# Kernel tuning notes

Measured on AMD Instinct MI355X. Metric: run time of the kernel, lower is better.

Reference implementation:

```python
import jax, jax.numpy as jnp
import numpy as np

D_MODEL = 1024
N_HEADS = 16
N_EXPERTS = 8
TOP_K = 2
EXPERT_HIDDEN = D_MODEL * 4 // N_EXPERTS  # 512, per MoELayer default


def layer_norm(x, g, b, eps=1e-5):
    mu = jnp.mean(x, axis=-1, keepdims=True)
    var = jnp.var(x, axis=-1, keepdims=True)
    return (x - mu) * jax.lax.rsqrt(var + eps) * g + b


def setup_inputs() -> dict:
    key = jax.random.key(0)
    ks = jax.random.split(key, 12)
    s = 1.0 / np.sqrt(D_MODEL)
    return {
        "x": jax.random.normal(ks[0], (2, 2048, D_MODEL), dtype=jnp.float32),
        "Wq": jax.random.normal(ks[1], (D_MODEL, D_MODEL), dtype=jnp.float32) * s,
        "Wk": jax.random.normal(ks[2], (D_MODEL, D_MODEL), dtype=jnp.float32) * s,
        "Wv": jax.random.normal(ks[3], (D_MODEL, D_MODEL), dtype=jnp.float32) * s,
        "Wo": jax.random.normal(ks[4], (D_MODEL, D_MODEL), dtype=jnp.float32) * s,
        "g1": jnp.ones((D_MODEL,), jnp.float32),
        "b1": jnp.zeros((D_MODEL,), jnp.float32),
        "g2": jnp.ones((D_MODEL,), jnp.float32),
        "b2": jnp.zeros((D_MODEL,), jnp.float32),
        "Wg": jax.random.normal(ks[5], (D_MODEL, N_EXPERTS), dtype=jnp.float32) * s,
        "W1": jax.random.normal(ks[6], (N_EXPERTS, D_MODEL, EXPERT_HIDDEN), dtype=jnp.float32) * s,
        "W2": jax.random.normal(ks[7], (N_EXPERTS, EXPERT_HIDDEN, D_MODEL), dtype=jnp.float32) * (1.0 / np.sqrt(EXPERT_HIDDEN)),
    }


def reference(x, Wq, Wk, Wv, Wo, g1, b1, g2, b2, Wg, W1, W2):
    B, S, D = x.shape
    H, dk = N_HEADS, D // N_HEADS

    # ---- pre-norm attention + residual (dropout = identity in eval) ----
    xn = layer_norm(x, g1, b1)
    q = (xn @ Wq).reshape(B, S, H, dk).transpose(0, 2, 1, 3)  # [B,H,S,dk]
    k = (xn @ Wk).reshape(B, S, H, dk).transpose(0, 2, 1, 3)
    v = (xn @ Wv).reshape(B, S, H, dk).transpose(0, 2, 1, 3)
    scores = jnp.einsum("bhqd,bhkd->bhqk", q, k) / np.sqrt(dk)
    attn = jax.nn.softmax(scores, axis=-1)
    o = jnp.einsum("bhqk,bhkd->bhqd", attn, v)
    o = o.transpose(0, 2, 1, 3).reshape(B, S, D) @ Wo
    x = x + o

    # ---- pre-norm MoE + residual ----
    xn2 = layer_norm(x, g2, b2)
    xf = xn2.reshape(B * S, D)  # [T, D]
    gate = xf @ Wg  # [T, E]
    topv, topi = jax.lax.top_k(gate, TOP_K)  # [T, K]
    probs = jax.nn.softmax(topv, axis=-1)    # softmax over top-k scores
    # dense combine weights [T, E] (top-k indices are distinct)
    cw = jnp.sum(jax.nn.one_hot(topi, N_EXPERTS, dtype=xf.dtype) * probs[..., None], axis=1)
    h = jax.nn.relu(jnp.einsum("td,edh->teh", xf, W1))  # [T,E,Hid]
    y = jnp.einsum("teh,ehd->ted", h, W2)               # [T,E,D]
    moe = jnp.einsum("ted,te->td", y, cw).reshape(B, S, D)
    return x + moe
```

## Files before the change

### kernel.cpp

```cpp
#include <hip/hip_runtime.h>

typedef __attribute__((ext_vector_type(8))) _Float16 f16x8;
typedef __attribute__((ext_vector_type(4))) _Float16 f16x4;
typedef __attribute__((ext_vector_type(2))) _Float16 f16x2;
typedef __attribute__((ext_vector_type(2))) __fp16 fp16x2_n;
typedef __attribute__((ext_vector_type(8))) short bf16x8;
typedef __attribute__((ext_vector_type(4))) float f32x4;
typedef __attribute__((ext_vector_type(4))) unsigned short u16x4;
typedef __attribute__((ext_vector_type(4))) float fx4;

#define D_MODEL 1024
#define N_HEADS 16
#define SEQ 2048
#define TOKENS 4096
#define N_EXP 8
#define EHID 512
#define LO_S 2048.0f
#define INV_LO (1.0f / 2048.0f)
#define QSCALE 0.18033688011112043f
#define DTHR 11.0f

__device__ inline unsigned short f2bf(float f) {
  union { float f; unsigned u; } v; v.f = f;
  unsigned u = v.u;
  return (unsigned short)((u + 0x7FFFu + ((u >> 16) & 1u)) >> 16);
}

__device__ inline void split16(float v, _Float16& h, _Float16& l) {
  h = (_Float16)v;
  l = (_Float16)((v - (float)h) * LO_S);
}

__device__ inline void split2(float a, float b, f16x2& h, f16x2& l) {
  fp16x2_n hn = __builtin_amdgcn_cvt_pkrtz(a, b);
  h = __builtin_bit_cast(f16x2, hn);
  fp16x2_n ln = __builtin_amdgcn_cvt_pkrtz((a - (float)h[0]) * LO_S, (b - (float)h[1]) * LO_S);
  l = __builtin_bit_cast(f16x2, ln);
}

__device__ inline void gload_lds16(const void* g, void* lds) {
  __builtin_amdgcn_global_load_lds((const __attribute__((address_space(1))) void*)g,
                                   (__attribute__((address_space(3))) void*)lds, 16, 0, 0);
}

__global__ __launch_bounds__(256) void prep_kernel(const float* __restrict__ Wq, const float* __restrict__ Wk,
                                                   const float* __restrict__ Wv, const float* __restrict__ Wo,
                                                   const float* __restrict__ W1, const float* __restrict__ W2,
                                                   _Float16* __restrict__ qkvh, _Float16* __restrict__ qkvl,
                                                   _Float16* __restrict__ woh, _Float16* __restrict__ wol,
                                                   unsigned short* __restrict__ W1T, unsigned short* __restrict__ W2T,
                                                   int* __restrict__ cnt, int* __restrict__ perm) {
  int b = blockIdx.x;
  if (b >= 12288) {
    int i = (b - 12288) * 256 + threadIdx.x;
    if (i < 8) cnt[i] = 0;
    if (i < 8704) perm[i] = 0;
    return;
  }
  __shared__ float tile[32][33];
  int tx = threadIdx.x & 31, ty = threadIdx.x >> 5;
  if (b < 4096) {
    int z = b >> 10, rem = b & 1023;
    int c0 = (rem & 31) * 32, r0 = (rem >> 5) * 32;
    const float* src = (z == 0) ? Wq : (z == 1) ? Wk : (z == 2) ? Wv : Wo;
    _Float16* dh = (z < 3) ? qkvh + (size_t)z * 1048576 : woh;
    _Float16* dl = (z < 3) ? qkvl + (size_t)z * 1048576 : wol;
    #pragma unroll
    for (int i = 0; i < 4; i++) tile[ty + 8*i][tx] = src[(size_t)(r0 + ty + 8*i) * 1024 + c0 + tx];
    __syncthreads();
    #pragma unroll
    for (int i = 0; i < 4; i++) {
      float v = tile[tx][ty + 8*i];
      _Float16 h, lo; split16(v, h, lo);
      size_t idx = (size_t)(c0 + ty + 8*i) * 1024 + r0 + tx;
      dh[idx] = h; dl[idx] = lo;
    }
  } else if (b < 8192) {
    int q = b - 4096, z = q >> 9, rem = q & 511;
    int c0 = (rem & 15) * 32, r0 = (rem >> 4) * 32;
    const float* src = W1 + (size_t)z * 524288;
    unsigned short* dst = W1T + (size_t)z * 524288;
    #pragma unroll
    for (int i = 0; i < 4; i++) tile[ty + 8*i][tx] = src[(size_t)(r0 + ty + 8*i) * 512 + c0 + tx];
    __syncthreads();
    #pragma unroll
    for (int i = 0; i < 4; i++) dst[(size_t)(c0 + ty + 8*i) * 1024 + r0 + tx] = f2bf(tile[tx][ty + 8*i]);
  } else {
    int q = b - 8192, z = q >> 9, rem = q & 511;
    int c0 = (rem & 31) * 32, r0 = (rem >> 5) * 32;
    const float* src = W2 + (size_t)z * 524288;
    unsigned short* dst = W2T + (size_t)z * 524288;
    #pragma unroll
    for (int i = 0; i < 4; i++) tile[ty + 8*i][tx] = src[(size_t)(r0 + ty + 8*i) * 1024 + c0 + tx];
    __syncthreads();
    #pragma unroll
    for (int i = 0; i < 4; i++) dst[(size_t)(c0 + ty + 8*i) * 512 + r0 + tx] = f2bf(tile[tx][ty + 8*i]);
  }
}

__global__ __launch_bounds__(256) void ln_f16s_kernel(const float* __restrict__ x, const float* __restrict__ g,
                                                      const float* __restrict__ b,
                                                      _Float16* __restrict__ xh, _Float16* __restrict__ xl) {
  int t = blockIdx.x, tid = threadIdx.x;
  const float* row = x + (size_t)t * D_MODEL;
  fx4 v = *(const fx4*)(row + tid * 4);
  float s = v[0] + v[1] + v[2] + v[3];
  float s2 = v[0]*v[0] + v[1]*v[1] + v[2]*v[2] + v[3]*v[3];
  #pragma unroll
  for (int off = 1; off < 64; off <<= 1) { s += __shfl_xor(s, off); s2 += __shfl_xor(s2, off); }
  __shared__ float red[8];
  int wv = tid >> 6, wl = tid & 63;
  if (wl == 0) { red[wv] = s; red[4 + wv] = s2; }
  __syncthreads();
  s = red[0] + red[1] + red[2] + red[3];
  s2 = red[4] + red[5] + red[6] + red[7];
  float mu = s * (1.f / 1024.f);
  float var = s2 * (1.f / 1024.f) - mu * mu;
  float rstd = rsqrtf(var + 1e-5f);
  int kk = tid * 4;
  f16x4 oh, ol;
  #pragma unroll
  for (int c = 0; c < 4; c++) {
    float y = (v[c] - mu) * rstd * g[kk + c] + b[kk + c];
    _Float16 h, lo; split16(y, h, lo);
    oh[c] = h; ol[c] = lo;
  }
  *(f16x4*)(xh + (size_t)t * D_MODEL + kk) = oh;
  *(f16x4*)(xl + (size_t)t * D_MODEL + kk) = ol;
}

__device__ inline void gemm128s(const _Float16* __restrict__ Ah, const _Float16* __restrict__ Al,
                                const _Float16* __restrict__ Bh, const _Float16* __restrict__ Bl,
                                int lda, int ldb, int K, int bm, int bn,
                                _Float16* lsbuf, f32x4 (&acc)[4][4], f32x4 (&accx)[4][4]) {
  const int tid = threadIdx.x, w = tid >> 6, l = tid & 63, lr = l & 15, lg = l >> 4;
  const int wr = (w >> 1) * 64, wc = (w & 1) * 64;
  int ca = (((tid & 3) ^ ((tid >> 3) & 3)) * 8);
  int ra0 = tid >> 2, ra1 = 64 + (tid >> 2);
  const _Float16* gA0 = Ah + (size_t)(bm + ra0) * lda + ca;
  const _Float16* gA1 = Ah + (size_t)(bm + ra1) * lda + ca;
  const _Float16* gA2 = Al + (size_t)(bm + ra0) * lda + ca;
  const _Float16* gA3 = Al + (size_t)(bm + ra1) * lda + ca;
  const _Float16* gB0 = Bh + (size_t)(bn + ra0) * ldb + ca;
  const _Float16* gB1 = Bh + (size_t)(bn + ra1) * ldb + ca;
  const _Float16* gB2 = Bl + (size_t)(bn + ra0) * ldb + ca;
  const _Float16* gB3 = Bl + (size_t)(bn + ra1) * ldb + ca;
  char* base = (char*)lsbuf;
  const int wo = w * 1024;
#define STAGE8(bb, ko) do { \
    gload_lds16(gA0 + (ko), (bb) + wo);         gload_lds16(gA1 + (ko), (bb) + 4096 + wo);  \
    gload_lds16(gA2 + (ko), (bb) + 8192 + wo);  gload_lds16(gA3 + (ko), (bb) + 12288 + wo); \
    gload_lds16(gB0 + (ko), (bb) + 16384 + wo); gload_lds16(gB1 + (ko), (bb) + 20480 + wo); \
    gload_lds16(gB2 + (ko), (bb) + 24576 + wo); gload_lds16(gB3 + (ko), (bb) + 28672 + wo); } while (0)
  STAGE8(base, 0);
  __syncthreads();
  const int swzB = ((lg ^ ((lr >> 1) & 3)) << 4);
  int cur = 0;
  for (int ko = 0; ko < K; ko += 32) {
    char* bR = base + cur * 32768;
    if (ko + 32 < K) STAGE8(base + (cur ^ 1) * 32768, ko + 32);
    f16x8 ah[4], al4[4], bh4[4], bl4[4];
    #pragma unroll
    for (int m = 0; m < 4; m++) {
      int roff = (wr + m * 16 + lr) * 64 + swzB;
      ah[m]  = *(const f16x8*)(bR + roff);
      al4[m] = *(const f16x8*)(bR + 8192 + roff);
    }
    #pragma unroll
    for (int n = 0; n < 4; n++) {
      int roff = (wc + n * 16 + lr) * 64 + swzB;
      bh4[n] = *(const f16x8*)(bR + 16384 + roff);
      bl4[n] = *(const f16x8*)(bR + 24576 + roff);
    }
    __builtin_amdgcn_s_setprio(1);
    #pragma unroll
    for (int m = 0; m < 4; m++)
      #pragma unroll
      for (int n = 0; n < 4; n++) {
        acc[m][n]  = __builtin_amdgcn_mfma_f32_16x16x32_f16(ah[m], bh4[n], acc[m][n], 0, 0, 0);
        accx[m][n] = __builtin_amdgcn_mfma_f32_16x16x32_f16(ah[m], bl4[n], accx[m][n], 0, 0, 0);
        accx[m][n] = __builtin_amdgcn_mfma_f32_16x16x32_f16(al4[m], bh4[n], accx[m][n], 0, 0, 0);
      }
    __builtin_amdgcn_s_setprio(0);
    __syncthreads();
    cur ^= 1;
  }
#undef STAGE8
}

__global__ __launch_bounds__(256) void gemm_qkv_kernel(const _Float16* __restrict__ xh, const _Float16* __restrict__ xl,
                                                       const _Float16* __restrict__ Wh, const _Float16* __restrict__ Wl,
                                                       _Float16* __restrict__ qh, _Float16* __restrict__ ql,
                                                       _Float16* __restrict__ kh, _Float16* __restrict__ kl,
                                                       _Float16* __restrict__ vh, _Float16* __restrict__ vl) {
  __shared__ _Float16 ls[32768];
  f32x4 acc[4][4] = {}, accx[4][4] = {};
  int bid = blockIdx.x;
  int sw = (bid & 7) * 96 + (bid >> 3);
  int bm = (sw & 31) * 128, bn = (sw >> 5) * 128;
  gemm128s(xh, xl, Wh, Wl, 1024, 1024, 1024, bm, bn, ls, acc, accx);
  const int tid = threadIdx.x, w = tid >> 6, l = tid & 63, lr = l & 15, lg = l >> 4;
  const int wr = (w >> 1) * 64, wc = (w & 1) * 64;
  #pragma unroll
  for (int m = 0; m < 4; m++) {
    int row0 = bm + wr + m * 16 + lg * 4;
    #pragma unroll
    for (int n = 0; n < 4; n++) {
      int col = bn + wc + n * 16 + lr;
      int mat = col >> 10;
      int c = col & 1023, h = c >> 6, d = c & 63;
      if (mat == 2) {
        int bb = row0 >> 11, ss = row0 & 2047;
        int tile = ss >> 5, kvs = ss & 31;
        f16x4 ph, pl;
        #pragma unroll
        for (int j = 0; j < 4; j++) {
          float v = acc[m][n][j] + accx[m][n][j] * INV_LO;
          _Float16 hh, ll; split16(v, hh, ll);
          ph[j] = hh; pl[j] = ll;
        }
        size_t base = ((size_t)(bb * N_HEADS + h) * 64 + tile) * 2048;
        int off = d * 32 + ((((kvs >> 3) ^ ((d >> 1) & 3)) << 3) | (kvs & 7));
        *(f16x4*)(vh + base + off) = ph;
        *(f16x4*)(vl + base + off) = pl;
      } else if (mat == 1) {
        #pragma unroll
        for (int j = 0; j < 4; j++) {
          float v = acc[m][n][j] + accx[m][n][j] * INV_LO;
          _Float16 hh, ll; split16(v, hh, ll);
          int t = row0 + j, bb = t >> 11, ss = t & 2047;
          int tile = ss >> 5, r = ss & 31;
          size_t base = ((size_t)(bb * N_HEADS + h) * 64 + tile) * 2048;
          int off = r * 64 + ((((d >> 3) ^ (r & 7)) << 3) | (d & 7));
          kh[base + off] = hh; kl[base + off] = ll;
        }
      } else {
        #pragma unroll
        for (int j = 0; j < 4; j++) {
          float v = (acc[m][n][j] + accx[m][n][j] * INV_LO) * QSCALE;
          _Float16 hh, ll; split16(v, hh, ll);
          int t = row0 + j, bb = t >> 11, ss = t & 2047;
          size_t idx = ((size_t)(bb * N_HEADS + h) * SEQ + ss) * 64 + d;
          qh[idx] = hh; ql[idx] = ll;
        }
      }
    }
  }
}

__global__ __launch_bounds__(256, 4) void flash_kernel(const _Float16* __restrict__ qhp, const _Float16* __restrict__ qlp,
                                                       const _Float16* __restrict__ khs, const _Float16* __restrict__ kls,
                                                       const _Float16* __restrict__ vhs, const _Float16* __restrict__ vls,
                                                       _Float16* __restrict__ oh, _Float16* __restrict__ ol) {
  __shared__ _Float16 lsKV[2][8192];
  __shared__ _Float16 lsP[4][2][512];
  int wgid = blockIdx.x;
  int xcd = wgid & 7, kk = wgid >> 3;
  int bh = xcd * 4 + (kk >> 5), qt = kk & 31;
  int tid = threadIdx.x, w = tid >> 6, l = tid & 63, lr = l & 15, lg = l >> 4;
  int q0 = qt * 64 + w * 16;
  const _Float16* qhb = qhp + (size_t)bh * SEQ * 64;
  const _Float16* qlb = qlp + (size_t)bh * SEQ * 64;
  f16x8 qfh[2], qfl[2];
  #pragma unroll
  for (int ks = 0; ks < 2; ks++) {
    size_t idx = (size_t)(q0 + lr) * 64 + ks * 32 + lg * 8;
    qfh[ks] = *(const f16x8*)(qhb + idx);
    qfl[ks] = *(const f16x8*)(qlb + idx);
  }
  const _Float16* splane = (w == 0) ? khs : (w == 1) ? kls : (w == 2) ? vhs : vls;
  const _Float16* sbase = splane + (size_t)bh * 131072 + l * 8;

  f32x4 acc[4] = {}, accx[4] = {};
  float mst = -1e30f, lstp = 0.f;

  {
    const _Float16* sp = sbase;
    _Float16* dd = &lsKV[0][w * 2048];
    gload_lds16(sp, dd); gload_lds16(sp + 512, dd + 512);
    gload_lds16(sp + 1024, dd + 1024); gload_lds16(sp + 1536, dd + 1536);
  }
  __syncthreads();

  for (int t = 0; t < 64; t++) {
    int bR = t & 1;
    if (t < 63) {
      const _Float16* sp = sbase + (size_t)(t + 1) * 2048;
      _Float16* dd = &lsKV[bR ^ 1][w * 2048];
      gload_lds16(sp, dd); gload_lds16(sp + 512, dd + 512);
      gload_lds16(sp + 1024, dd + 1024); gload_lds16(sp + 1536, dd + 1536);
    }
    char* bufB = (char*)&lsKV[bR][0];

    f32x4 s[2] = {}, sx[2] = {};
    #pragma unroll
    for (int ks = 0; ks < 2; ks++) {
      f16x8 kfh[2], kfl[2];
      #pragma unroll
      for (int m = 0; m < 2; m++) {
        int off = (m * 16 + lr) * 128 + (((ks * 4 + lg) ^ (lr & 7)) << 4);
        kfh[m] = *(const f16x8*)(bufB + off);
        kfl[m] = *(const f16x8*)(bufB + 4096 + off);
      }
      __builtin_amdgcn_s_setprio(1);
      #pragma unroll
      for (int m = 0; m < 2; m++) {
        s[m]  = __builtin_amdgcn_mfma_f32_16x16x32_f16(kfh[m], qfh[ks], s[m], 0, 0, 0);
        sx[m] = __builtin_amdgcn_mfma_f32_16x16x32_f16(kfh[m], qfl[ks], sx[m], 0, 0, 0);
        sx[m] = __builtin_amdgcn_mfma_f32_16x16x32_f16(kfl[m], qfh[ks], sx[m], 0, 0, 0);
      }
      __builtin_amdgcn_s_setprio(0);
    }

    float tm = -3e38f;
    #pragma unroll
    for (int m = 0; m < 2; m++)
      #pragma unroll
      for (int j = 0; j < 4; j++) {
        s[m][j] += sx[m][j] * INV_LO;
        tm = fmaxf(tm, s[m][j]);
      }
    if (!__all(tm - mst <= DTHR)) {
      tm = fmaxf(tm, __shfl_xor(tm, 16));
      tm = fmaxf(tm, __shfl_xor(tm, 32));
      float mnew = fmaxf(mst, tm);
      float corr = exp2f(mst - mnew);
      #pragma unroll
      for (int m2 = 0; m2 < 4; m2++)
        #pragma unroll
        for (int j = 0; j < 4; j++) { acc[m2][j] *= corr; accx[m2][j] *= corr; }
      lstp *= corr;
      mst = mnew;
    }
    #pragma unroll
    for (int m = 0; m < 2; m++) {
      #pragma unroll
      for (int j = 0; j < 4; j++) {
        float p = exp2f(s[m][j] - mst);
        lstp += p;
        s[m][j] = p;
      }
      f16x2 h01, h23, l01, l23;
      split2(s[m][0], s[m][1], h01, l01);
      split2(s[m][2], s[m][3], h23, l23);
      f16x4 ph, pl;
      ph[0] = h01[0]; ph[1] = h01[1]; ph[2] = h23[0]; ph[3] = h23[1];
      pl[0] = l01[0]; pl[1] = l01[1]; pl[2] = l23[0]; pl[3] = l23[1];
      int boff = lr * 64 + ((((m * 2 + (lg >> 1)) ^ ((lr >> 1) & 3)) << 4) | ((lg & 1) * 8));
      *(f16x4*)((char*)&lsP[w][0][0] + boff) = ph;
      *(f16x4*)((char*)&lsP[w][1][0] + boff) = pl;
    }

    int poff = lr * 64 + ((lg ^ ((lr >> 1) & 3)) << 4);
    f16x8 pfh = *(const f16x8*)((char*)&lsP[w][0][0] + poff);
    f16x8 pfl = *(const f16x8*)((char*)&lsP[w][1][0] + poff);
    __builtin_amdgcn_s_setprio(1);
    #pragma unroll
    for (int m2 = 0; m2 < 4; m2++) {
      int voff = (m2 * 16 + lr) * 64 + ((lg ^ ((lr >> 1) & 3)) << 4);
      f16x8 vfh = *(const f16x8*)(bufB + 8192 + voff);
      f16x8 vfl = *(const f16x8*)(bufB + 12288 + voff);
      acc[m2]  = __builtin_amdgcn_mfma_f32_16x16x32_f16(vfh, pfh, acc[m2], 0, 0, 0);
      accx[m2] = __builtin_amdgcn_mfma_f32_16x16x32_f16(vfh, pfl, accx[m2], 0, 0, 0);
      accx[m2] = __builtin_amdgcn_mfma_f32_16x16x32_f16(vfl, pfh, accx[m2], 0, 0, 0);
    }
    __builtin_amdgcn_s_setprio(0);
    __syncthreads();
  }

  float lst = lstp + __shfl_xor(lstp, 16);
  lst += __shfl_xor(lst, 32);
  float inv = 1.f / lst;
  int b = bh >> 4, h = bh & 15;
  int tkn = b * SEQ + q0 + lr;
  #pragma unroll
  for (int m2 = 0; m2 < 4; m2++) {
    f16x4 ph, pl;
    #pragma unroll
    for (int j = 0; j < 4; j++) {
      float o = (acc[m2][j] + accx[m2][j] * INV_LO) * inv;
      _Float16 hh, ll; split16(o, hh, ll);
      ph[j] = hh; pl[j] = ll;
    }
    size_t idx = (size_t)tkn * D_MODEL + h * 64 + m2 * 16 + lg * 4;
    *(f16x4*)(oh + idx) = ph;
    *(f16x4*)(ol + idx) = pl;
  }
}

__global__ __launch_bounds__(256) void gemm_oproj_kernel(const _Float16* __restrict__ ah, const _Float16* __restrict__ al,
                                                         const _Float16* __restrict__ Wh, const _Float16* __restrict__ Wl,
                                                         const float* __restrict__ x, float* __restrict__ out) {
  __shared__ _Float16 ls[32768];
  f32x4 acc[4][4] = {}, accx[4][4] = {};
  int bid = blockIdx.x;
  int sw = (bid & 7) * 32 + (bid >> 3);
  int bm = (sw & 31) * 128, bn = (sw >> 5) * 128;
  gemm128s(ah, al, Wh, Wl, 1024, 1024, 1024, bm, bn, ls, acc, accx);
  const int tid = threadIdx.x, w = tid >> 6, l = tid & 63, lr = l & 15, lg = l >> 4;
  const int wr = (w >> 1) * 64, wc = (w & 1) * 64;
  #pragma unroll
  for (int m = 0; m < 4; m++) {
    int row0 = bm + wr + m * 16 + lg * 4;
    #pragma unroll
    for (int n = 0; n < 4; n++) {
      int col = bn + wc + n * 16 + lr;
      #pragma unroll
      for (int j = 0; j < 4; j++) {
        size_t idx = (size_t)(row0 + j) * D_MODEL + col;
        out[idx] = (acc[m][n][j] + accx[m][n][j] * INV_LO) + x[idx];
      }
    }
  }
}

__global__ __launch_bounds__(256) void gate_kernel(const float* __restrict__ x1, const float* __restrict__ Wg,
                                                   const float* __restrict__ g2, const float* __restrict__ b2,
                                                   unsigned short* __restrict__ xn2,
                                                   int* __restrict__ cnt, int* __restrict__ topi,
                                                   float* __restrict__ topw) {
  int t = blockIdx.x * 4 + (threadIdx.x >> 6);
  int l = threadIdx.x & 63;
  const float* row = x1 + (size_t)t * D_MODEL;
  fx4 v[4];
  float s = 0.f, s2 = 0.f;
  #pragma unroll
  for (int i = 0; i < 4; i++) {
    v[i] = *(const fx4*)(row + l * 16 + i * 4);
    #pragma unroll
    for (int c = 0; c < 4; c++) { s += v[i][c]; s2 += v[i][c] * v[i][c]; }
  }
  #pragma unroll
  for (int off = 1; off < 64; off <<= 1) { s += __shfl_xor(s, off); s2 += __shfl_xor(s2, off); }
  float mu = s * (1.f / 1024.f);
  float var = s2 * (1.f / 1024.f) - mu * mu;
  float rstd = rsqrtf(var + 1e-5f);
  float a8[8] = {0,0,0,0,0,0,0,0};
  #pragma unroll
  for (int i = 0; i < 4; i++) {
    u16x4 ox;
    #pragma unroll
    for (int c = 0; c < 4; c++) {
      int kk = l * 16 + i * 4 + c;
      float xv = (v[i][c] - mu) * rstd * g2[kk] + b2[kk];
      ox[c] = f2bf(xv);
      const float* wr_ = Wg + (size_t)kk * 8;
      fx4 wa = *(const fx4*)wr_;
      fx4 wb = *(const fx4*)(wr_ + 4);
      a8[0] += xv * wa[0]; a8[1] += xv * wa[1]; a8[2] += xv * wa[2]; a8[3] += xv * wa[3];
      a8[4] += xv * wb[0]; a8[5] += xv * wb[1]; a8[6] += xv * wb[2]; a8[7] += xv * wb[3];
    }
    *(u16x4*)(xn2 + (size_t)t * D_MODEL + l * 16 + i * 4) = ox;
  }
  #pragma unroll
  for (int e = 0; e < 8; e++)
    #pragma unroll
    for (int off = 1; off < 64; off <<= 1) a8[e] += __shfl_xor(a8[e], off);
  if (l == 0) {
    int i0 = 0; float v0 = a8[0];
    #pragma unroll
    for (int e = 1; e < 8; e++) if (a8[e] > v0) { v0 = a8[e]; i0 = e; }
    int i1 = -1; float v1 = -3.4e38f;
    #pragma unroll
    for (int e = 0; e < 8; e++) if (e != i0 && a8[e] > v1) { v1 = a8[e]; i1 = e; }
    float p0 = 1.f / (1.f + __expf(v1 - v0));
    topi[t * 2] = i0; topi[t * 2 + 1] = i1;
    topw[t * 2] = p0; topw[t * 2 + 1] = 1.f - p0;
    atomicAdd(&cnt[i0], 1); atomicAdd(&cnt[i1], 1);
  }
}

__global__ __launch_bounds__(256) void scatter_kernel(const int* __restrict__ topi, const int* __restrict__ cnt,
                                                      int* __restrict__ perm, int* __restrict__ slot_of) {
  int e = blockIdx.x, tid = threadIdx.x;
  __shared__ int basesh;
  __shared__ int wsum[4];
  if (tid == 0) {
    int a = 0;
    for (int i = 0; i < e; i++) a += ((cnt[i] + 63) >> 6) << 6;
    basesh = a;
  }
  __syncthreads();
  for (int seg = 0; seg < 8192; seg += 256) {
    int a = seg + tid;
    int match = (topi[a] == e) ? 1 : 0;
    unsigned long long bal = __ballot(match);
    int wl = tid & 63, wv = tid >> 6;
    int lanepre = __popcll(bal & ((1ULL << wl) - 1ULL));
    if (wl == 0) wsum[wv] = __popcll(bal);
    __syncthreads();
    int wpre = 0;
    for (int i = 0; i < wv; i++) wpre += wsum[i];
    int total = wsum[0] + wsum[1] + wsum[2] + wsum[3];
    if (match) {
      int pos = basesh + wpre + lanepre;
      perm[pos] = a >> 1;
      slot_of[a] = pos;
    }
    __syncthreads();
    if (tid == 0) basesh += total;
    __syncthreads();
  }
}

__global__ __launch_bounds__(512) void moe_ffn_kernel(const unsigned short* __restrict__ xn2,
                                                      const unsigned short* __restrict__ W1T,
                                                      const unsigned short* __restrict__ W2T,
                                                      const int* __restrict__ cnt,
                                                      const int* __restrict__ perm,
                                                      float* __restrict__ y) {
  int bid = blockIdx.x;
  int e = -1, lt = bid, off = 0;
  for (int i = 0; i < 8; i++) {
    int nt = (cnt[i] + 63) >> 6;
    if (lt < nt) { e = i; break; }
    lt -= nt; off += nt << 6;
  }
  if (e < 0) return;
  int slot0 = off + lt * 64;

  __shared__ int t_sh[64];
  __shared__ unsigned short lsX[64 * 128];
  __shared__ unsigned short hsh[64 * 264];
  int tid = threadIdx.x, w = tid >> 6, l = tid & 63, lr = l & 15, lg = l >> 4;
  if (tid < 64) t_sh[tid] = perm[slot0 + tid];
  __syncthreads();

  const unsigned short* W1e = W1T + (size_t)e * EHID * D_MODEL;
  const unsigned short* W2e = W2T + (size_t)e * D_MODEL * EHID;

  f32x4 acc2[4][8] = {};
  for (int h = 0; h < 2; h++) {
    f32x4 acc1[4][2] = {};
    for (int kc = 0; kc < 8; kc++) {
      __syncthreads();
      #pragma unroll
      for (int L = 0; L < 2; L++) {
        int u = tid + 512 * L;
        int r = u >> 4, sp = u & 15;
        int cs = (sp & 8) | ((sp & 7) ^ (r & 7));
        gload_lds16(xn2 + (size_t)t_sh[r] * D_MODEL + kc * 128 + cs * 8, (char*)lsX + u * 16);
      }
      __syncthreads();
      #pragma unroll
      for (int kst = 0; kst < 4; kst++) {
        bf16x8 a[4];
        #pragma unroll
        for (int m = 0; m < 4; m++) {
          int row = m * 16 + lr;
          int slot = kst * 4 + lg;
          int cs = (slot & 8) | ((slot & 7) ^ (row & 7));
          a[m] = *(const bf16x8*)((char*)lsX + row * 256 + cs * 16);
        }
        int ko = kc * 128 + kst * 32;
        #pragma unroll
        for (int n = 0; n < 2; n++) {
          bf16x8 bb = *(const bf16x8*)(W1e + (size_t)(h * 256 + w * 32 + n * 16 + lr) * D_MODEL + ko + lg * 8);
          #pragma unroll
          for (int m = 0; m < 4; m++)
            acc1[m][n] = __builtin_amdgcn_mfma_f32_16x16x32_bf16(a[m], bb, acc1[m][n], 0, 0, 0);
        }
      }
    }
    __syncthreads();
    #pragma unroll
    for (int m = 0; m < 4; m++)
      #pragma unroll
      for (int n = 0; n < 2; n++)
        #pragma unroll
        for (int j = 0; j < 4; j++)
          hsh[(m*16 + lg*4 + j) * 264 + w * 32 + n * 16 + lr] = f2bf(fmaxf(acc1[m][n][j], 0.f));
    __syncthreads();
    for (int k2 = 0; k2 < 256; k2 += 32) {
      bf16x8 a2[4];
      #pragma unroll
      for (int m = 0; m < 4; m++) a2[m] = *(const bf16x8*)(hsh + (m*16 + lr) * 264 + k2 + lg * 8);
      #pragma unroll
      for (int n = 0; n < 8; n++) {
        bf16x8 bb = *(const bf16x8*)(W2e + (size_t)(w * 128 + n * 16 + lr) * EHID + h * 256 + k2 + lg * 8);
        #pragma unroll
        for (int m = 0; m < 4; m++)
          acc2[m][n] = __builtin_amdgcn_mfma_f32_16x16x32_bf16(a2[m], bb, acc2[m][n], 0, 0, 0);
      }
    }
  }
  #pragma unroll
  for (int m = 0; m < 4; m++)
    #pragma unroll
    for (int j = 0; j < 4; j++) {
      int r = m * 16 + lg * 4 + j;
      #pragma unroll
      for (int n = 0; n < 8; n++)
        y[(size_t)(slot0 + r) * D_MODEL + w * 128 + n * 16 + lr] = acc2[m][n][j];
    }
}

__global__ __launch_bounds__(256) void combine_kernel(const float* __restrict__ y, const int* __restrict__ slot_of,
                                                      const float* __restrict__ topw, float* __restrict__ out) {
  int t = blockIdx.x * 4 + (threadIdx.x >> 6);
  int l = threadIdx.x & 63;
  int s0 = slot_of[t * 2], s1 = slot_of[t * 2 + 1];
  float w0 = topw[t * 2], w1 = topw[t * 2 + 1];
  const float* y0 = y + (size_t)s0 * D_MODEL + l * 16;
  const float* y1 = y + (size_t)s1 * D_MODEL + l * 16;
  float* o = out + (size_t)t * D_MODEL + l * 16;
  #pragma unroll
  for (int i = 0; i < 4; i++) {
    fx4 av = *(const fx4*)(y0 + i * 4);
    fx4 bv = *(const fx4*)(y1 + i * 4);
    fx4 d = *(const fx4*)(o + i * 4);
    #pragma unroll
    for (int j = 0; j < 4; j++) d[j] += w0 * av[j] + w1 * bv[j];
    *(fx4*)(o + i * 4) = d;
  }
}

#define MB (1u << 20)
extern "C" void kernel_launch(void* const* d_in, const int* in_sizes, int n_in,
                              void* d_out, int out_size, void* d_ws, size_t ws_size,
                              hipStream_t stream) {
  const float* x  = (const float*)d_in[0];
  const float* Wq = (const float*)d_in[1];
  const float* Wk = (const float*)d_in[2];
  const float* Wv = (const float*)d_in[3];
  const float* Wo = (const float*)d_in[4];
  const float* g1 = (const float*)d_in[5];
  const float* b1 = (const float*)d_in[6];
  const float* g2 = (const float*)d_in[7];
  const float* b2 = (const float*)d_in[8];
  const float* Wg = (const float*)d_in[9];
  const float* W1 = (const float*)d_in[10];
  const float* W2 = (const float*)d_in[11];
  float* out = (float*)d_out;

  char* ws = (char*)d_ws;
  _Float16* xn1h = (_Float16*)(ws + 0*MB);
  _Float16* xn1l = (_Float16*)(ws + 8*MB);
  _Float16* Wqkh = (_Float16*)(ws + 16*MB);
  _Float16* Wqkl = (_Float16*)(ws + 22*MB);
  _Float16* Woh  = (_Float16*)(ws + 28*MB);
  _Float16* Wol  = (_Float16*)(ws + 30*MB);
  _Float16* qhb  = (_Float16*)(ws + 32*MB);
  _Float16* qlb  = (_Float16*)(ws + 40*MB);
  _Float16* khb  = (_Float16*)(ws + 48*MB);
  _Float16* klb  = (_Float16*)(ws + 56*MB);
  _Float16* vhb  = (_Float16*)(ws + 64*MB);
  _Float16* vlb  = (_Float16*)(ws + 72*MB);
  unsigned short* xn2 = (unsigned short*)(ws + 80*MB);
  unsigned short* W1T = (unsigned short*)(ws + 88*MB);
  unsigned short* W2T = (unsigned short*)(ws + 96*MB);
  char* misc = ws + 104*MB;
  int*   topi    = (int*)(misc);
  float* topw    = (float*)(misc + 32768);
  int*   slot_of = (int*)(misc + 65536);
  int*   cnt     = (int*)(misc + 98304);
  int*   perm    = (int*)(misc + 98368);
  float* ybuf    = (float*)(ws + 32*MB);
  _Float16* attnh = xn1h;
  _Float16* attnl = xn1l;

  prep_kernel<<<12322, 256, 0, stream>>>(Wq, Wk, Wv, Wo, W1, W2, Wqkh, Wqkl, Woh, Wol, W1T, W2T, cnt, perm);

  ln_f16s_kernel<<<TOKENS, 256, 0, stream>>>(x, g1, b1, xn1h, xn1l);
  gemm_qkv_kernel<<<768, 256, 0, stream>>>(xn1h, xn1l, Wqkh, Wqkl, qhb, qlb, khb, klb, vhb, vlb);
  flash_kernel<<<1024, 256, 0, stream>>>(qhb, qlb, khb, klb, vhb, vlb, attnh, attnl);
  gemm_oproj_kernel<<<256, 256, 0, stream>>>(attnh, attnl, Woh, Wol, x, out);

  gate_kernel<<<1024, 256, 0, stream>>>(out, Wg, g2, b2, xn2, cnt, topi, topw);
  scatter_kernel<<<8, 256, 0, stream>>>(topi, cnt, perm, slot_of);
  moe_ffn_kernel<<<136, 512, 0, stream>>>(xn2, W1T, W2T, cnt, perm, ybuf);
  combine_kernel<<<1024, 256, 0, stream>>>(ybuf, slot_of, topw, out);

  (void)in_sizes; (void)n_in; (void)out_size; (void)ws_size;
}
```

Baseline: 529.7 us.

## Merge LN into prep kernel; load GEMM B and flash V directly from global

```diff
diff --git a/kernel.cpp b/kernel.cpp
--- a/kernel.cpp
+++ b/kernel.cpp
@@ -43,14 +43,47 @@
                                    (__attribute__((address_space(3))) void*)lds, 16, 0, 0);
 }
 
-__global__ __launch_bounds__(256) void prep_kernel(const float* __restrict__ Wq, const float* __restrict__ Wk,
-                                                   const float* __restrict__ Wv, const float* __restrict__ Wo,
-                                                   const float* __restrict__ W1, const float* __restrict__ W2,
-                                                   _Float16* __restrict__ qkvh, _Float16* __restrict__ qkvl,
-                                                   _Float16* __restrict__ woh, _Float16* __restrict__ wol,
-                                                   unsigned short* __restrict__ W1T, unsigned short* __restrict__ W2T,
-                                                   int* __restrict__ cnt, int* __restrict__ perm) {
-  int b = blockIdx.x;
+__global__ __launch_bounds__(256) void prep_ln_kernel(const float* __restrict__ x, const float* __restrict__ g1,
+                                                      const float* __restrict__ b1,
+                                                      _Float16* __restrict__ xh, _Float16* __restrict__ xl,
+                                                      const float* __restrict__ Wq, const float* __restrict__ Wk,
+                                                      const float* __restrict__ Wv, const float* __restrict__ Wo,
+                                                      const float* __restrict__ W1, const float* __restrict__ W2,
+                                                      _Float16* __restrict__ qkvh, _Float16* __restrict__ qkvl,
+                                                      _Float16* __restrict__ woh, _Float16* __restrict__ wol,
+                                                      unsigned short* __restrict__ W1T, unsigned short* __restrict__ W2T,
+                                                      int* __restrict__ cnt, int* __restrict__ perm) {
+  int bb = blockIdx.x;
+  if (bb < 4096) {
+    int t = bb, tid = threadIdx.x;
+    const float* row = x + (size_t)t * D_MODEL;
+    fx4 v = *(const fx4*)(row + tid * 4);
+    float s = v[0] + v[1] + v[2] + v[3];
+    float s2 = v[0]*v[0] + v[1]*v[1] + v[2]*v[2] + v[3]*v[3];
+    #pragma unroll
+    for (int off = 1; off < 64; off <<= 1) { s += __shfl_xor(s, off); s2 += __shfl_xor(s2, off); }
+    __shared__ float red[8];
+    int wv = tid >> 6, wl = tid & 63;
+    if (wl == 0) { red[wv] = s; red[4 + wv] = s2; }
+    __syncthreads();
+    s = red[0] + red[1] + red[2] + red[3];
+    s2 = red[4] + red[5] + red[6] + red[7];
+    float mu = s * (1.f / 1024.f);
+    float var = s2 * (1.f / 1024.f) - mu * mu;
+    float rstd = rsqrtf(var + 1e-5f);
+    int kk = tid * 4;
+    f16x4 oh, ol;
+    #pragma unroll
+    for (int c = 0; c < 4; c++) {
+      float y = (v[c] - mu) * rstd * g1[kk + c] + b1[kk + c];
+      _Float16 h, lo; split16(y, h, lo);
+      oh[c] = h; ol[c] = lo;
+    }
+    *(f16x4*)(xh + (size_t)t * D_MODEL + kk) = oh;
+    *(f16x4*)(xl + (size_t)t * D_MODEL + kk) = ol;
+    return;
+  }
+  int b = bb - 4096;
   if (b >= 12288) {
     int i = (b - 12288) * 256 + threadIdx.x;
     if (i < 8) cnt[i] = 0;
@@ -96,37 +129,6 @@
     #pragma unroll
     for (int i = 0; i < 4; i++) dst[(size_t)(c0 + ty + 8*i) * 512 + r0 + tx] = f2bf(tile[tx][ty + 8*i]);
   }
-}
-
-__global__ __launch_bounds__(256) void ln_f16s_kernel(const float* __restrict__ x, const float* __restrict__ g,
-                                                      const float* __restrict__ b,
-                                                      _Float16* __restrict__ xh, _Float16* __restrict__ xl) {
-  int t = blockIdx.x, tid = threadIdx.x;
-  const float* row = x + (size_t)t * D_MODEL;
-  fx4 v = *(const fx4*)(row + tid * 4);
-  float s = v[0] + v[1] + v[2] + v[3];
-  float s2 = v[0]*v[0] + v[1]*v[1] + v[2]*v[2] + v[3]*v[3];
-  #pragma unroll
-  for (int off = 1; off < 64; off <<= 1) { s += __shfl_xor(s, off); s2 += __shfl_xor(s2, off); }
-  __shared__ float red[8];
-  int wv = tid >> 6, wl = tid & 63;
-  if (wl == 0) { red[wv] = s; red[4 + wv] = s2; }
-  __syncthreads();
-  s = red[0] + red[1] + red[2] + red[3];
-  s2 = red[4] + red[5] + red[6] + red[7];
-  float mu = s * (1.f / 1024.f);
-  float var = s2 * (1.f / 1024.f) - mu * mu;
-  float rstd = rsqrtf(var + 1e-5f);
-  int kk = tid * 4;
-  f16x4 oh, ol;
-  #pragma unroll
-  for (int c = 0; c < 4; c++) {
-    float y = (v[c] - mu) * rstd * g[kk + c] + b[kk + c];
-    _Float16 h, lo; split16(y, h, lo);
-    oh[c] = h; ol[c] = lo;
-  }
-  *(f16x4*)(xh + (size_t)t * D_MODEL + kk) = oh;
-  *(f16x4*)(xl + (size_t)t * D_MODEL + kk) = ol;
 }
 
 __device__ inline void gemm128s(const _Float16* __restrict__ Ah, const _Float16* __restrict__ Al,
@@ -141,37 +143,33 @@
   const _Float16* gA1 = Ah + (size_t)(bm + ra1) * lda + ca;
   const _Float16* gA2 = Al + (size_t)(bm + ra0) * lda + ca;
   const _Float16* gA3 = Al + (size_t)(bm + ra1) * lda + ca;
-  const _Float16* gB0 = Bh + (size_t)(bn + ra0) * ldb + ca;
-  const _Float16* gB1 = Bh + (size_t)(bn + ra1) * ldb + ca;
-  const _Float16* gB2 = Bl + (size_t)(bn + ra0) * ldb + ca;
-  const _Float16* gB3 = Bl + (size_t)(bn + ra1) * ldb + ca;
+  const _Float16* gBh = Bh + (size_t)(bn + wc + lr) * ldb + lg * 8;
+  const _Float16* gBl = Bl + (size_t)(bn + wc + lr) * ldb + lg * 8;
   char* base = (char*)lsbuf;
   const int wo = w * 1024;
-#define STAGE8(bb, ko) do { \
-    gload_lds16(gA0 + (ko), (bb) + wo);         gload_lds16(gA1 + (ko), (bb) + 4096 + wo);  \
-    gload_lds16(gA2 + (ko), (bb) + 8192 + wo);  gload_lds16(gA3 + (ko), (bb) + 12288 + wo); \
-    gload_lds16(gB0 + (ko), (bb) + 16384 + wo); gload_lds16(gB1 + (ko), (bb) + 20480 + wo); \
-    gload_lds16(gB2 + (ko), (bb) + 24576 + wo); gload_lds16(gB3 + (ko), (bb) + 28672 + wo); } while (0)
-  STAGE8(base, 0);
+#define STAGE4(bb_, ko) do { \
+    gload_lds16(gA0 + (ko), (bb_) + wo);        gload_lds16(gA1 + (ko), (bb_) + 4096 + wo); \
+    gload_lds16(gA2 + (ko), (bb_) + 8192 + wo); gload_lds16(gA3 + (ko), (bb_) + 12288 + wo); } while (0)
+  STAGE4(base, 0);
   __syncthreads();
   const int swzB = ((lg ^ ((lr >> 1) & 3)) << 4);
   int cur = 0;
   for (int ko = 0; ko < K; ko += 32) {
-    char* bR = base + cur * 32768;
-    if (ko + 32 < K) STAGE8(base + (cur ^ 1) * 32768, ko + 32);
-    f16x8 ah[4], al4[4], bh4[4], bl4[4];
+    char* bR = base + cur * 16384;
+    f16x8 bh4[4], bl4[4];
+    #pragma unroll
+    for (int n = 0; n < 4; n++) {
+      bh4[n] = *(const f16x8*)(gBh + (size_t)(n * 16) * ldb + ko);
+      bl4[n] = *(const f16x8*)(gBl + (size_t)(n * 16) * ldb + ko);
+    }
+    if (ko + 32 < K) STAGE4(base + (cur ^ 1) * 16384, ko + 32);
+    f16x8 ah[4], al4[4];
     #pragma unroll
     for (int m = 0; m < 4; m++) {
       int roff = (wr + m * 16 + lr) * 64 + swzB;
       ah[m]  = *(const f16x8*)(bR + roff);
       al4[m] = *(const f16x8*)(bR + 8192 + roff);
     }
-    #pragma unroll
-    for (int n = 0; n < 4; n++) {
-      int roff = (wc + n * 16 + lr) * 64 + swzB;
-      bh4[n] = *(const f16x8*)(bR + 16384 + roff);
-      bl4[n] = *(const f16x8*)(bR + 24576 + roff);
-    }
     __builtin_amdgcn_s_setprio(1);
     #pragma unroll
     for (int m = 0; m < 4; m++)
@@ -185,7 +183,7 @@
     __syncthreads();
     cur ^= 1;
   }
-#undef STAGE8
+#undef STAGE4
 }
 
 __global__ __launch_bounds__(256) void gemm_qkv_kernel(const _Float16* __restrict__ xh, const _Float16* __restrict__ xl,
@@ -193,7 +191,7 @@
                                                        _Float16* __restrict__ qh, _Float16* __restrict__ ql,
                                                        _Float16* __restrict__ kh, _Float16* __restrict__ kl,
                                                        _Float16* __restrict__ vh, _Float16* __restrict__ vl) {
-  __shared__ _Float16 ls[32768];
+  __shared__ _Float16 ls[16384];
   f32x4 acc[4][4] = {}, accx[4][4] = {};
   int bid = blockIdx.x;
   int sw = (bid & 7) * 96 + (bid >> 3);
@@ -211,7 +209,6 @@
       int c = col & 1023, h = c >> 6, d = c & 63;
       if (mat == 2) {
         int bb = row0 >> 11, ss = row0 & 2047;
-        int tile = ss >> 5, kvs = ss & 31;
         f16x4 ph, pl;
         #pragma unroll
         for (int j = 0; j < 4; j++) {
@@ -219,10 +216,9 @@
           _Float16 hh, ll; split16(v, hh, ll);
           ph[j] = hh; pl[j] = ll;
         }
-        size_t base = ((size_t)(bb * N_HEADS + h) * 64 + tile) * 2048;
-        int off = d * 32 + ((((kvs >> 3) ^ ((d >> 1) & 3)) << 3) | (kvs & 7));
-        *(f16x4*)(vh + base + off) = ph;
-        *(f16x4*)(vl + base + off) = pl;
+        size_t base = ((size_t)(bb * N_HEADS + h) * 64 + d) * 2048 + ss;
+        *(f16x4*)(vh + base) = ph;
+        *(f16x4*)(vl + base) = pl;
       } else if (mat == 1) {
         #pragma unroll
         for (int j = 0; j < 4; j++) {
@@ -248,11 +244,11 @@
   }
 }
 
-__global__ __launch_bounds__(256, 4) void flash_kernel(const _Float16* __restrict__ qhp, const _Float16* __restrict__ qlp,
+__global__ __launch_bounds__(256, 3) void flash_kernel(const _Float16* __restrict__ qhp, const _Float16* __restrict__ qlp,
                                                        const _Float16* __restrict__ khs, const _Float16* __restrict__ kls,
-                                                       const _Float16* __restrict__ vhs, const _Float16* __restrict__ vls,
+                                                       const _Float16* __restrict__ vhp, const _Float16* __restrict__ vlp,
                                                        _Float16* __restrict__ oh, _Float16* __restrict__ ol) {
-  __shared__ _Float16 lsKV[2][8192];
+  __shared__ _Float16 lsK[2][4096];
   __shared__ _Float16 lsP[4][2][512];
   int wgid = blockIdx.x;
   int xcd = wgid & 7, kk = wgid >> 3;
@@ -268,29 +264,28 @@
     qfh[ks] = *(const f16x8*)(qhb + idx);
     qfl[ks] = *(const f16x8*)(qlb + idx);
   }
-  const _Float16* splane = (w == 0) ? khs : (w == 1) ? kls : (w == 2) ? vhs : vls;
-  const _Float16* sbase = splane + (size_t)bh * 131072 + l * 8;
+  const _Float16* ksrc = ((w & 1) ? kls : khs) + (size_t)bh * 131072 + (w >> 1) * 1024 + l * 8;
+  const _Float16* vhb = vhp + (size_t)bh * 131072;
+  const _Float16* vlb = vlp + (size_t)bh * 131072;
 
   f32x4 acc[4] = {}, accx[4] = {};
   float mst = -1e30f, lstp = 0.f;
 
   {
-    const _Float16* sp = sbase;
-    _Float16* dd = &lsKV[0][w * 2048];
-    gload_lds16(sp, dd); gload_lds16(sp + 512, dd + 512);
-    gload_lds16(sp + 1024, dd + 1024); gload_lds16(sp + 1536, dd + 1536);
+    _Float16* dd = &lsK[0][(w & 1) * 2048 + (w >> 1) * 1024];
+    gload_lds16(ksrc, dd); gload_lds16(ksrc + 512, dd + 512);
   }
   __syncthreads();
 
   for (int t = 0; t < 64; t++) {
     int bR = t & 1;
+    int kv0 = t * 32;
     if (t < 63) {
-      const _Float16* sp = sbase + (size_t)(t + 1) * 2048;
-      _Float16* dd = &lsKV[bR ^ 1][w * 2048];
+      const _Float16* sp = ksrc + (size_t)(t + 1) * 2048;
+      _Float16* dd = &lsK[bR ^ 1][(w & 1) * 2048 + (w >> 1) * 1024];
       gload_lds16(sp, dd); gload_lds16(sp + 512, dd + 512);
-      gload_lds16(sp + 1024, dd + 1024); gload_lds16(sp + 1536, dd + 1536);
-    }
-    char* bufB = (char*)&lsKV[bR][0];
+    }
+    char* bufB = (char*)&lsK[bR][0];
 
     f32x4 s[2] = {}, sx[2] = {};
     #pragma unroll
@@ -310,6 +305,14 @@
         sx[m] = __builtin_amdgcn_mfma_f32_16x16x32_f16(kfl[m], qfh[ks], sx[m], 0, 0, 0);
       }
       __builtin_amdgcn_s_setprio(0);
+    }
+
+    f16x8 vfh[4], vfl[4];
+    #pragma unroll
+    for (int m2 = 0; m2 < 4; m2++) {
+      size_t va = (size_t)(m2 * 16 + lr) * 2048 + kv0 + lg * 8;
+      vfh[m2] = *(const f16x8*)(vhb + va);
+      vfl[m2] = *(const f16x8*)(vlb + va);
     }
 
     float tm = -3e38f;
@@ -357,12 +360,9 @@
     __builtin_amdgcn_s_setprio(1);
     #pragma unroll
     for (int m2 = 0; m2 < 4; m2++) {
-      int voff = (m2 * 16 + lr) * 64 + ((lg ^ ((lr >> 1) & 3)) << 4);
-      f16x8 vfh = *(const f16x8*)(bufB + 8192 + voff);
-      f16x8 vfl = *(const f16x8*)(bufB + 12288 + voff);
-      acc[m2]  = __builtin_amdgcn_mfma_f32_16x16x32_f16(vfh, pfh, acc[m2], 0, 0, 0);
-      accx[m2] = __builtin_amdgcn_mfma_f32_16x16x32_f16(vfh, pfl, accx[m2], 0, 0, 0);
-      accx[m2] = __builtin_amdgcn_mfma_f32_16x16x32_f16(vfl, pfh, accx[m2], 0, 0, 0);
+      acc[m2]  = __builtin_amdgcn_mfma_f32_16x16x32_f16(vfh[m2], pfh, acc[m2], 0, 0, 0);
+      accx[m2] = __builtin_amdgcn_mfma_f32_16x16x32_f16(vfh[m2], pfl, accx[m2], 0, 0, 0);
+      accx[m2] = __builtin_amdgcn_mfma_f32_16x16x32_f16(vfl[m2], pfh, accx[m2], 0, 0, 0);
     }
     __builtin_amdgcn_s_setprio(0);
     __syncthreads();
@@ -391,7 +391,7 @@
 __global__ __launch_bounds__(256) void gemm_oproj_kernel(const _Float16* __restrict__ ah, const _Float16* __restrict__ al,
                                                          const _Float16* __restrict__ Wh, const _Float16* __restrict__ Wl,
                                                          const float* __restrict__ x, float* __restrict__ out) {
-  __shared__ _Float16 ls[32768];
+  __shared__ _Float16 ls[16384];
   f32x4 acc[4][4] = {}, accx[4][4] = {};
   int bid = blockIdx.x;
   int sw = (bid & 7) * 32 + (bid >> 3);
@@ -659,9 +659,10 @@
   _Float16* attnh = xn1h;
   _Float16* attnl = xn1l;
 
-  prep_kernel<<<12322, 256, 0, stream>>>(Wq, Wk, Wv, Wo, W1, W2, Wqkh, Wqkl, Woh, Wol, W1T, W2T, cnt, perm);
-
-  ln_f16s_kernel<<<TOKENS, 256, 0, stream>>>(x, g1, b1, xn1h, xn1l);
+  prep_ln_kernel<<<16419, 256, 0, stream>>>(x, g1, b1, xn1h, xn1l,
+                                            Wq, Wk, Wv, Wo, W1, W2,
+                                            Wqkh, Wqkl, Woh, Wol, W1T, W2T, cnt, perm);
+
   gemm_qkv_kernel<<<768, 256, 0, stream>>>(xn1h, xn1l, Wqkh, Wqkl, qhb, qlb, khb, klb, vhb, vlb);
   flash_kernel<<<1024, 256, 0, stream>>>(qhb, qlb, khb, klb, vhb, vlb, attnh, attnl);
   gemm_oproj_kernel<<<256, 256, 0, stream>>>(attnh, attnl, Woh, Wol, x, out);
```

After: 767.0 us. 44.8% more time.
